# Kernel optimization log

Hardware: AMD Instinct MI355X
Metric: run time of the kernel (lower is better)

## Reference

```python
import jax, jax.numpy as jnp
import numpy as np
from jax.scipy.special import logsumexp

B = 2048       # anchors
P = 4          # positives per anchor (constant -> ragged list collapses to [B,P])
D = 256        # embed dim
N_NEG = 32768  # shared negative bank
TEMPERATURE = 0.05
ALPHA = 0.1
EPS = 1e-12    # F.normalize eps


def _l2norm(x):
    n = jnp.sqrt(jnp.sum(x * x, axis=-1, keepdims=True))
    return x / jnp.maximum(n, EPS)


def setup_inputs() -> dict:
    key = jax.random.key(0)
    k1, k2, k3 = jax.random.split(key, 3)
    return {
        "anchor_embeddings": jax.random.normal(k1, (B, D), jnp.float32),
        "positive_embeddings": jax.random.normal(k2, (B * P, D), jnp.float32),
        "negative_embeddings": jax.random.normal(k3, (N_NEG, D), jnp.float32),
        "num_positives_per_anchor": jnp.full((B,), P, dtype=jnp.int32),
    }


def reference(anchor_embeddings, positive_embeddings, negative_embeddings,
              num_positives_per_anchor):
    a = _l2norm(anchor_embeddings)                       # [B, D]
    p = _l2norm(positive_embeddings).reshape(B, P, D)    # [B, P, D]
    n = _l2norm(negative_embeddings)                     # [N, D]

    pos_sim = jnp.einsum("bd,bpd->bp", a, p) / TEMPERATURE   # [B, P]
    neg_sim = jnp.einsum("bd,nd->bn", a, n) / TEMPERATURE    # [B, N]  (dominant traffic)
    neg_lse = logsumexp(neg_sim, axis=1)                     # [B]

    # per-(anchor, positive) CE with label 0 over logits [pos_j, neg_sim_i]:
    # loss = logsumexp([pos_j, neg...]) - pos_j = logaddexp(pos_j, neg_lse_i) - pos_j
    pair_loss = jnp.logaddexp(pos_sim, neg_lse[:, None]) - pos_sim   # [B, P]
    counts = num_positives_per_anchor
    pair_mask = jnp.arange(P)[None, :] < counts[:, None]             # [B, P]
    total = jnp.sum(jnp.where(pair_mask, pair_loss, 0.0))

    # weighted-positive term (only for anchors with num_pos > 1)
    w = jax.nn.softmax(pos_sim, axis=1)                  # [B, P]
    wps = jnp.sum(w * pos_sim, axis=1)                   # [B]
    wloss = jnp.logaddexp(wps, neg_lse) - wps            # [B]
    total = total + ALPHA * jnp.sum(jnp.where(counts > 1, wloss, 0.0))

    return total / B
```

## Files before the change

### kernel.cpp

```cpp
#include <hip/hip_runtime.h>
#include <math.h>

constexpr int   B       = 2048;
constexpr int   P       = 4;
constexpr int   D       = 256;
constexpr int   NNEG    = 32768;
constexpr int   NTILES  = NNEG / 64;
constexpr float TEMP    = 0.05f;
constexpr float ALPHA   = 0.1f;
constexpr float EPS     = 1e-12f;
constexpr float INV_T   = 1.0f / TEMP;
constexpr float SCALE_Q = 28.853900817779268f;

typedef float f32x4 __attribute__((ext_vector_type(4)));
typedef int   i32x8 __attribute__((ext_vector_type(8)));

__device__ inline unsigned short f2bf(float f) {
  unsigned int u = __float_as_uint(f);
  u = (u + 0x7fffu + ((u >> 16) & 1u)) >> 16;
  return (unsigned short)u;
}
__device__ inline float bf2f(unsigned short u) {
  return __uint_as_float((unsigned int)u << 16);
}

__device__ inline float ror16_add(float v) {
  int x;
  x = __builtin_amdgcn_update_dpp(0, __float_as_int(v), 0x121, 0xf, 0xf, true);
  v += __int_as_float(x);
  x = __builtin_amdgcn_update_dpp(0, __float_as_int(v), 0x122, 0xf, 0xf, true);
  v += __int_as_float(x);
  x = __builtin_amdgcn_update_dpp(0, __float_as_int(v), 0x124, 0xf, 0xf, true);
  v += __int_as_float(x);
  x = __builtin_amdgcn_update_dpp(0, __float_as_int(v), 0x128, 0xf, 0xf, true);
  v += __int_as_float(x);
  return v;
}


constexpr int NPANEL = (B + NNEG) / 16;
constexpr int LSTR   = 264;

__global__ __launch_bounds__(256) void prep_kernel(
    const float* __restrict__ a,
    const float* __restrict__ pzx,
    const float* __restrict__ n,
    unsigned char* __restrict__ a_f8,
    unsigned char* __restrict__ n_f8,
    float* __restrict__ pos_sim,
    float* __restrict__ loss_acc,
    unsigned int* __restrict__ ticket) {
  if (blockIdx.x == 0 && threadIdx.x == 0) { *loss_acc = 0.0f; *ticket = 0u; }
  const int id   = blockIdx.x;
  const int tid  = threadIdx.x;
  const int wave = tid >> 6;
  const int lane = tid & 63;

  if (id < NPANEL) {
    __shared__ __align__(16) unsigned short sm[16 * LSTR];
    const bool isA = (id < B / 16);
    const float* src; unsigned char* dst; int prow; float post;
    if (isA) { src = a; dst = a_f8; prow = id;          post = SCALE_Q; }
    else     { src = n; dst = n_f8; prow = id - B / 16; post = 1.0f; }

#pragma unroll
    for (int rr = 0; rr < 4; rr++) {
      const int r = wave * 4 + rr;
      float4 v = ((const float4*)(src + ((size_t)prow * 16 + r) * D))[lane];
      float ss = v.x * v.x + v.y * v.y + v.z * v.z + v.w * v.w;
#pragma unroll
      for (int off = 32; off > 0; off >>= 1) ss += __shfl_xor(ss, off, 64);
      float inv = post / fmaxf(sqrtf(ss), EPS);
      ushort4 o;
      o.x = f2bf(v.x * inv); o.y = f2bf(v.y * inv);
      o.z = f2bf(v.z * inv); o.w = f2bf(v.w * inv);
      *(ushort4*)&sm[r * LSTR + lane * 4] = o;
    }
    __syncthreads();

    const int o = tid * 16;
    int r, k0;
    if (isA) {
      r  = (o >> 4) & 15;
      k0 = (o >> 11) * 128 + ((o >> 8) & 3) * 32 + ((o >> 10) & 1) * 16;
    } else {
      r  = (o >> 5) & 15;
      k0 = (o >> 11) * 128 + ((o >> 9) & 3) * 32 + (o & 16);
    }
    const unsigned short* s1 = &sm[r * LSTR + k0];
    uint4 ov;
    {
      int w0 = __builtin_amdgcn_cvt_pk_fp8_f32(bf2f(s1[0]),  bf2f(s1[1]),  0,  false);
      w0     = __builtin_amdgcn_cvt_pk_fp8_f32(bf2f(s1[2]),  bf2f(s1[3]),  w0, true);
      int w1 = __builtin_amdgcn_cvt_pk_fp8_f32(bf2f(s1[4]),  bf2f(s1[5]),  0,  false);
      w1     = __builtin_amdgcn_cvt_pk_fp8_f32(bf2f(s1[6]),  bf2f(s1[7]),  w1, true);
      int w2 = __builtin_amdgcn_cvt_pk_fp8_f32(bf2f(s1[8]),  bf2f(s1[9]),  0,  false);
      w2     = __builtin_amdgcn_cvt_pk_fp8_f32(bf2f(s1[10]), bf2f(s1[11]), w2, true);
      int w3 = __builtin_amdgcn_cvt_pk_fp8_f32(bf2f(s1[12]), bf2f(s1[13]), 0,  false);
      w3     = __builtin_amdgcn_cvt_pk_fp8_f32(bf2f(s1[14]), bf2f(s1[15]), w3, true);
      ov.x = (unsigned)w0; ov.y = (unsigned)w1;
      ov.z = (unsigned)w2; ov.w = (unsigned)w3;
    }
    *(uint4*)(dst + (size_t)prow * 4096 + tid * 16) = ov;
  } else {
    int pw = (id - NPANEL) * 4 + wave;
    if (pw >= B * P) return;
    int b = pw >> 2;
    float4 av = ((const float4*)(a + (size_t)b * D))[lane];
    float4 pv = ((const float4*)(pzx + (size_t)pw * D))[lane];
    float d  = av.x * pv.x + av.y * pv.y + av.z * pv.z + av.w * pv.w;
    float sa = av.x * av.x + av.y * av.y + av.z * av.z + av.w * av.w;
    float sp = pv.x * pv.x + pv.y * pv.y + pv.z * pv.z + pv.w * pv.w;
#pragma unroll
    for (int off = 32; off > 0; off >>= 1) {
      d  += __shfl_xor(d, off, 64);
      sa += __shfl_xor(sa, off, 64);
      sp += __shfl_xor(sp, off, 64);
    }
    if (lane == 0) {
      float inva = 1.0f / fmaxf(sqrtf(sa), EPS);
      float invp = 1.0f / fmaxf(sqrtf(sp), EPS);
      pos_sim[pw] = d * inva * invp * INV_T;
    }
  }
}

__global__ __launch_bounds__(512, 4) void negsim_mfma_kernel(
    const unsigned char* __restrict__ Af,
    const unsigned char* __restrict__ Nf,
    float* __restrict__ part_s) {
  __shared__ __align__(16) unsigned char As[4 * 4096];
  __shared__ float part_l[2][8][64];

  const int tid  = threadIdx.x;
  const int wave = tid >> 6;
  const int lane = tid & 63;

  const int id     = blockIdx.x;
  const int ngroup = id & 15;
  const int mblk   = id >> 4;
  const int m0     = mblk * 64;

#pragma unroll
  for (int t = 0; t < 2; t++) {
    const int s = wave * 2 + t;
    __builtin_amdgcn_global_load_lds(
        (const __attribute__((address_space(1))) unsigned int*)
            (Af + (size_t)(m0 >> 4) * 4096 + s * 1024 + lane * 16),
        (__attribute__((address_space(3))) unsigned int*)(As + s * 1024 + lane * 16),
        16, 0, 0);
  }

  const unsigned char* Bw = Nf + (size_t)(ngroup * 128 + wave * 2) * 4096 + lane * 32;

  i32x8 bfP0 = *(const i32x8*)(Bw);
  i32x8 bfP1 = *(const i32x8*)(Bw + 4096);
  i32x8 bfP2 = *(const i32x8*)(Bw + 2048);
  i32x8 bfP3 = *(const i32x8*)(Bw + 4096 + 2048);

  __syncthreads();

  const int aoff = lane * 16;

#define DO_ITER(B0, B1, B2, B3, PB, ITEXPR)                                    \
  {                                                                            \
    f32x4 acc[4][2] = {};                                                      \
    _Pragma("unroll")                                                          \
    for (int mi = 0; mi < 4; mi++) {                                           \
      int4 lo = *(const int4*)&As[mi * 4096 + aoff];                           \
      int4 hi = *(const int4*)&As[mi * 4096 + 1024 + aoff];                    \
      i32x8 af;                                                                \
      af[0] = lo.x; af[1] = lo.y; af[2] = lo.z; af[3] = lo.w;                  \
      af[4] = hi.x; af[5] = hi.y; af[6] = hi.z; af[7] = hi.w;                  \
      acc[mi][0] = __builtin_amdgcn_mfma_scale_f32_16x16x128_f8f6f4(           \
          af, B0, acc[mi][0], 0, 0, 0, 0x7f7f7f7f, 0, 0x7f7f7f7f);             \
      acc[mi][1] = __builtin_amdgcn_mfma_scale_f32_16x16x128_f8f6f4(           \
          af, B1, acc[mi][1], 0, 0, 0, 0x7f7f7f7f, 0, 0x7f7f7f7f);             \
    }                                                                          \
    _Pragma("unroll")                                                          \
    for (int mi = 0; mi < 4; mi++) {                                           \
      int4 lo = *(const int4*)&As[mi * 4096 + 2048 + aoff];                    \
      int4 hi = *(const int4*)&As[mi * 4096 + 2048 + 1024 + aoff];             \
      i32x8 af;                                                                \
      af[0] = lo.x; af[1] = lo.y; af[2] = lo.z; af[3] = lo.w;                  \
      af[4] = hi.x; af[5] = hi.y; af[6] = hi.z; af[7] = hi.w;                  \
      acc[mi][0] = __builtin_amdgcn_mfma_scale_f32_16x16x128_f8f6f4(           \
          af, B2, acc[mi][0], 0, 0, 0, 0x7f7f7f7f, 0, 0x7f7f7f7f);             \
      acc[mi][1] = __builtin_amdgcn_mfma_scale_f32_16x16x128_f8f6f4(           \
          af, B3, acc[mi][1], 0, 0, 0, 0x7f7f7f7f, 0, 0x7f7f7f7f);             \
    }                                                                          \
    _Pragma("unroll")                                                          \
    for (int mi = 0; mi < 4; mi++) {                                           \
      _Pragma("unroll")                                                        \
      for (int rr = 0; rr < 4; rr++) {                                         \
        float e = __builtin_amdgcn_exp2f(acc[mi][0][rr]) +                     \
                  __builtin_amdgcn_exp2f(acc[mi][1][rr]);                      \
        e = ror16_add(e);                                                      \
        if ((lane & 15) == 0)                                                  \
          part_l[PB][wave][mi * 16 + (lane >> 4) * 4 + rr] = e;                \
      }                                                                        \
    }                                                                          \
    asm volatile("s_waitcnt lgkmcnt(0)" ::: "memory");                         \
    __builtin_amdgcn_sched_barrier(0);                                         \
    __builtin_amdgcn_s_barrier();                                              \
    __builtin_amdgcn_sched_barrier(0);                                         \
    if (tid < 256) {                                                           \
      const int u4  = tid >> 6;                                                \
      const int row = tid & 63;                                                \
      float s64 = part_l[PB][2 * u4][row] + part_l[PB][2 * u4 + 1][row];       \
      part_s[(size_t)(m0 + row) * NTILES + (ngroup * 32 + (ITEXPR) * 4 + u4)]  \
          = s64;                                                               \
    }                                                                          \
  }

#pragma unroll 1
  for (int t = 0; t < 4; t++) {
    const int it0 = 2 * t;
    const unsigned char* Bq  = Bw + (size_t)(it0 + 1) * 16 * 4096;
    const unsigned char* Bpn = Bw + (size_t)((it0 + 2) & 7) * 16 * 4096;

    i32x8 bfQ0 = *(const i32x8*)(Bq);
    i32x8 bfQ1 = *(const i32x8*)(Bq + 4096);
    i32x8 bfQ2 = *(const i32x8*)(Bq + 2048);
    i32x8 bfQ3 = *(const i32x8*)(Bq + 4096 + 2048);

    DO_ITER(bfP0, bfP1, bfP2, bfP3, 0, it0)

    bfP0 = *(const i32x8*)(Bpn);
    bfP1 = *(const i32x8*)(Bpn + 4096);
    bfP2 = *(const i32x8*)(Bpn + 2048);
    bfP3 = *(const i32x8*)(Bpn + 4096 + 2048);

    DO_ITER(bfQ0, bfQ1, bfQ2, bfQ3, 1, it0 + 1)
  }
#undef DO_ITER
}

__global__ void loss_kernel(const float* __restrict__ part_s,
                            const float* __restrict__ pos_sim,
                            const int* __restrict__ counts,
                            float* __restrict__ loss_acc,
                            unsigned int* __restrict__ ticket,
                            float* __restrict__ out) {
  const int tid = threadIdx.x;
  const int b   = blockIdx.x * 16 + (tid >> 4);
  const int sub = tid & 15;
  const float* ps = part_s + (size_t)b * NTILES;
  float s = 0.0f;
#pragma unroll
  for (int i = 0; i < NTILES / 16; i++) s += ps[sub + i * 16];
  s += __shfl_xor(s, 1, 64);
  s += __shfl_xor(s, 2, 64);
  s += __shfl_xor(s, 4, 64);
  s += __shfl_xor(s, 8, 64);

  float acc = 0.0f;
  if (sub == 0) {
    float L = logf(s);
    float p0 = pos_sim[b * P + 0], p1 = pos_sim[b * P + 1];
    float p2 = pos_sim[b * P + 2], p3 = pos_sim[b * P + 3];
    int cnt = counts[b];
    float pj[P] = {p0, p1, p2, p3};
#pragma unroll
    for (int jj = 0; jj < P; jj++) {
      if (jj < cnt) {
        float hi = fmaxf(pj[jj], L), lo = fminf(pj[jj], L);
        acc += hi + log1pf(__expf(lo - hi)) - pj[jj];
      }
    }
    float mp = fmaxf(fmaxf(p0, p1), fmaxf(p2, p3));
    float e0 = __expf(p0 - mp), e1 = __expf(p1 - mp);
    float e2 = __expf(p2 - mp), e3 = __expf(p3 - mp);
    float se = e0 + e1 + e2 + e3;
    float wps = (e0 * p0 + e1 * p1 + e2 * p2 + e3 * p3) / se;
    if (cnt > 1) {
      float hi = fmaxf(wps, L), lo = fminf(wps, L);
      acc += ALPHA * (hi + log1pf(__expf(lo - hi)) - wps);
    }
  }
#pragma unroll
  for (int off = 32; off > 0; off >>= 1) acc += __shfl_xor(acc, off, 64);
  __shared__ float sa[4];
  int wid = tid >> 6, lane = tid & 63;
  if (lane == 0) sa[wid] = acc;
  __syncthreads();
  if (tid == 0) {
    atomicAdd(loss_acc, sa[0] + sa[1] + sa[2] + sa[3]);
    __threadfence();
    unsigned int t = atomicAdd(ticket, 1u);
    if (t == (unsigned int)gridDim.x - 1u) {
      float total = atomicAdd(loss_acc, 0.0f);
      out[0] = total / (float)B;
    }
  }
}

extern "C" void kernel_launch(void* const* d_in, const int* in_sizes, int n_in,
                              void* d_out, int out_size, void* d_ws,
                              size_t ws_size, hipStream_t stream) {
  const float* anc    = (const float*)d_in[0];
  const float* pos    = (const float*)d_in[1];
  const float* neg    = (const float*)d_in[2];
  const int*   counts = (const int*)d_in[3];
  float* out = (float*)d_out;

  unsigned char* a_f8 = (unsigned char*)d_ws;
  unsigned char* n_f8 = a_f8 + (size_t)B * D;
  float* part_s  = (float*)(n_f8 + (size_t)NNEG * D);
  float* pos_sim = part_s + (size_t)B * NTILES;
  float* loss_acc = pos_sim + B * P;
  unsigned int* ticket = (unsigned int*)(loss_acc + 1);

  prep_kernel<<<NPANEL + B * P / 4, 256, 0, stream>>>(
      anc, pos, neg, a_f8, n_f8, pos_sim, loss_acc, ticket);

  negsim_mfma_kernel<<<512, 512, 0, stream>>>(a_f8, n_f8, part_s);

  loss_kernel<<<B / 16, 256, 0, stream>>>(part_s, pos_sim, counts,
                                          loss_acc, ticket, out);
}
```

Measured before the change: 123.9 us.

## Keep anchor fragments in registers and drop LDS reduction barriers in negsim kernel

The anchor FP8 layout now matches the negative layout, so each wave loads its A fragments directly from global memory into registers instead of staging them through LDS. The per-iteration LDS cross-wave reduction and block barrier are removed. Each wave writes its own 32-column partial sums straight to part_s, which doubles the partial-sum buffer and the work done by loss_kernel. Grid is halved, each block covers twice as many negatives, and the launch bound drops to 2 blocks per CU to make room for the extra registers. The cost is higher register pressure and more global stores.

```diff
diff --git a/kernel.cpp b/kernel.cpp
--- a/kernel.cpp
+++ b/kernel.cpp
@@ -5,7 +5,7 @@
 constexpr int   P       = 4;
 constexpr int   D       = 256;
 constexpr int   NNEG    = 32768;
-constexpr int   NTILES  = NNEG / 64;
+constexpr int   NTILES  = NNEG / 32;
 constexpr float TEMP    = 0.05f;
 constexpr float ALPHA   = 0.1f;
 constexpr float EPS     = 1e-12f;
@@ -58,10 +58,9 @@
 
   if (id < NPANEL) {
     __shared__ __align__(16) unsigned short sm[16 * LSTR];
-    const bool isA = (id < B / 16);
     const float* src; unsigned char* dst; int prow; float post;
-    if (isA) { src = a; dst = a_f8; prow = id;          post = SCALE_Q; }
-    else     { src = n; dst = n_f8; prow = id - B / 16; post = 1.0f; }
+    if (id < B / 16) { src = a; dst = a_f8; prow = id;          post = SCALE_Q; }
+    else             { src = n; dst = n_f8; prow = id - B / 16; post = 1.0f; }
 
 #pragma unroll
     for (int rr = 0; rr < 4; rr++) {
@@ -78,15 +77,9 @@
     }
     __syncthreads();
 
-    const int o = tid * 16;
-    int r, k0;
-    if (isA) {
-      r  = (o >> 4) & 15;
-      k0 = (o >> 11) * 128 + ((o >> 8) & 3) * 32 + ((o >> 10) & 1) * 16;
-    } else {
-      r  = (o >> 5) & 15;
-      k0 = (o >> 11) * 128 + ((o >> 9) & 3) * 32 + (o & 16);
-    }
+    const int o  = tid * 16;
+    const int r  = (o >> 5) & 15;
+    const int k0 = (o >> 11) * 128 + ((o >> 9) & 3) * 32 + (o & 31);
     const unsigned short* s1 = &sm[r * LSTR + k0];
     uint4 ov;
     {
@@ -125,70 +118,56 @@
   }
 }
 
-__global__ __launch_bounds__(512, 4) void negsim_mfma_kernel(
+__global__ __launch_bounds__(512, 2) void negsim_mfma_kernel(
     const unsigned char* __restrict__ Af,
     const unsigned char* __restrict__ Nf,
     float* __restrict__ part_s) {
-  __shared__ __align__(16) unsigned char As[4 * 4096];
-  __shared__ float part_l[2][8][64];
-
   const int tid  = threadIdx.x;
   const int wave = tid >> 6;
   const int lane = tid & 63;
 
   const int id     = blockIdx.x;
-  const int ngroup = id & 15;
-  const int mblk   = id >> 4;
+  const int ngroup = id & 7;
+  const int mblk   = id >> 3;
   const int m0     = mblk * 64;
 
-#pragma unroll
-  for (int t = 0; t < 2; t++) {
-    const int s = wave * 2 + t;
-    __builtin_amdgcn_global_load_lds(
-        (const __attribute__((address_space(1))) unsigned int*)
-            (Af + (size_t)(m0 >> 4) * 4096 + s * 1024 + lane * 16),
-        (__attribute__((address_space(3))) unsigned int*)(As + s * 1024 + lane * 16),
-        16, 0, 0);
-  }
-
-  const unsigned char* Bw = Nf + (size_t)(ngroup * 128 + wave * 2) * 4096 + lane * 32;
+  const unsigned char* Ap = Af + (size_t)(m0 >> 4) * 4096 + lane * 32;
+  i32x8 af[4][2];
+#pragma unroll
+  for (int mi = 0; mi < 4; mi++)
+#pragma unroll
+    for (int h = 0; h < 2; h++)
+      af[mi][h] = *(const i32x8*)(Ap + (size_t)mi * 4096 + h * 2048);
+
+  const unsigned char* Bw =
+      Nf + (size_t)(ngroup * 256 + wave * 2) * 4096 + lane * 32;
+
+  const int rowbase = m0 + (lane >> 4) * 4;
+  const int colbase = ngroup * 128 + wave;
 
   i32x8 bfP0 = *(const i32x8*)(Bw);
   i32x8 bfP1 = *(const i32x8*)(Bw + 4096);
   i32x8 bfP2 = *(const i32x8*)(Bw + 2048);
   i32x8 bfP3 = *(const i32x8*)(Bw + 4096 + 2048);
 
-  __syncthreads();
-
-  const int aoff = lane * 16;
-
-#define DO_ITER(B0, B1, B2, B3, PB, ITEXPR)                                    \
+#define DO_ITER(B0, B1, B2, B3, ITEXPR)                                        \
   {                                                                            \
     f32x4 acc[4][2] = {};                                                      \
     _Pragma("unroll")                                                          \
     for (int mi = 0; mi < 4; mi++) {                                           \
-      int4 lo = *(const int4*)&As[mi * 4096 + aoff];                           \
-      int4 hi = *(const int4*)&As[mi * 4096 + 1024 + aoff];                    \
-      i32x8 af;                                                                \
-      af[0] = lo.x; af[1] = lo.y; af[2] = lo.z; af[3] = lo.w;                  \
-      af[4] = hi.x; af[5] = hi.y; af[6] = hi.z; af[7] = hi.w;                  \
       acc[mi][0] = __builtin_amdgcn_mfma_scale_f32_16x16x128_f8f6f4(           \
-          af, B0, acc[mi][0], 0, 0, 0, 0x7f7f7f7f, 0, 0x7f7f7f7f);             \
+          af[mi][0], B0, acc[mi][0], 0, 0, 0, 0x7f7f7f7f, 0, 0x7f7f7f7f);      \
       acc[mi][1] = __builtin_amdgcn_mfma_scale_f32_16x16x128_f8f6f4(           \
-          af, B1, acc[mi][1], 0, 0, 0, 0x7f7f7f7f, 0, 0x7f7f7f7f);             \
+          af[mi][0], B1, acc[mi][1], 0, 0, 0, 0x7f7f7f7f, 0, 0x7f7f7f7f);      \
     }                                                                          \
     _Pragma("unroll")                                                          \
     for (int mi = 0; mi < 4; mi++) {                                           \
-      int4 lo = *(const int4*)&As[mi * 4096 + 2048 + aoff];                    \
-      int4 hi = *(const int4*)&As[mi * 4096 + 2048 + 1024 + aoff];             \
-      i32x8 af;                                                                \
-      af[0] = lo.x; af[1] = lo.y; af[2] = lo.z; af[3] = lo.w;                  \
-      af[4] = hi.x; af[5] = hi.y; af[6] = hi.z; af[7] = hi.w;                  \
       acc[mi][0] = __builtin_amdgcn_mfma_scale_f32_16x16x128_f8f6f4(           \
-          af, B2, acc[mi][0], 0, 0, 0, 0x7f7f7f7f, 0, 0x7f7f7f7f);             \
+          af[mi][1], B2, acc[mi][0], 0, 0, 0, 0x7f7f7f7f, 0, 0x7f7f7f7f);      \
       acc[mi][1] = __builtin_amdgcn_mfma_scale_f32_16x16x128_f8f6f4(           \
-          af, B3, acc[mi][1], 0, 0, 0, 0x7f7f7f7f, 0, 0x7f7f7f7f);             \
+          af[mi][1], B3, acc[mi][1], 0, 0, 0, 0x7f7f7f7f, 0, 0x7f7f7f7f);      \
     }                                                                          \
+    const int col_ = colbase + (ITEXPR) * 8;                                   \
     _Pragma("unroll")                                                          \
     for (int mi = 0; mi < 4; mi++) {                                           \
       _Pragma("unroll")                                                        \
@@ -197,41 +176,30 @@
                   __builtin_amdgcn_exp2f(acc[mi][1][rr]);                      \
         e = ror16_add(e);                                                      \
         if ((lane & 15) == 0)                                                  \
-          part_l[PB][wave][mi * 16 + (lane >> 4) * 4 + rr] = e;                \
+          part_s[(size_t)(rowbase + mi * 16 + rr) * NTILES + col_] = e;        \
       }                                                                        \
     }                                                                          \
-    asm volatile("s_waitcnt lgkmcnt(0)" ::: "memory");                         \
-    __builtin_amdgcn_sched_barrier(0);                                         \
-    __builtin_amdgcn_s_barrier();                                              \
-    __builtin_amdgcn_sched_barrier(0);                                         \
-    if (tid < 256) {                                                           \
-      const int u4  = tid >> 6;                                                \
-      const int row = tid & 63;                                                \
-      float s64 = part_l[PB][2 * u4][row] + part_l[PB][2 * u4 + 1][row];       \
-      part_s[(size_t)(m0 + row) * NTILES + (ngroup * 32 + (ITEXPR) * 4 + u4)]  \
-          = s64;                                                               \
-    }                                                                          \
   }
 
 #pragma unroll 1
-  for (int t = 0; t < 4; t++) {
+  for (int t = 0; t < 8; t++) {
     const int it0 = 2 * t;
     const unsigned char* Bq  = Bw + (size_t)(it0 + 1) * 16 * 4096;
-    const unsigned char* Bpn = Bw + (size_t)((it0 + 2) & 7) * 16 * 4096;
+    const unsigned char* Bpn = Bw + (size_t)((it0 + 2) & 15) * 16 * 4096;
 
     i32x8 bfQ0 = *(const i32x8*)(Bq);
     i32x8 bfQ1 = *(const i32x8*)(Bq + 4096);
     i32x8 bfQ2 = *(const i32x8*)(Bq + 2048);
     i32x8 bfQ3 = *(const i32x8*)(Bq + 4096 + 2048);
 
-    DO_ITER(bfP0, bfP1, bfP2, bfP3, 0, it0)
+    DO_ITER(bfP0, bfP1, bfP2, bfP3, it0)
 
     bfP0 = *(const i32x8*)(Bpn);
     bfP1 = *(const i32x8*)(Bpn + 4096);
     bfP2 = *(const i32x8*)(Bpn + 2048);
     bfP3 = *(const i32x8*)(Bpn + 4096 + 2048);
 
-    DO_ITER(bfQ0, bfQ1, bfQ2, bfQ3, 1, it0 + 1)
+    DO_ITER(bfQ0, bfQ1, bfQ2, bfQ3, it0 + 1)
   }
 #undef DO_ITER
 }
@@ -314,7 +282,7 @@
   prep_kernel<<<NPANEL + B * P / 4, 256, 0, stream>>>(
       anc, pos, neg, a_f8, n_f8, pos_sim, loss_acc, ticket);
 
-  negsim_mfma_kernel<<<512, 512, 0, stream>>>(a_f8, n_f8, part_s);
+  negsim_mfma_kernel<<<256, 512, 0, stream>>>(a_f8, n_f8, part_s);
 
   loss_kernel<<<B / 16, 256, 0, stream>>>(part_s, pos_sim, counts,
                                           loss_acc, ticket, out);
```

Result: slower. 134.8 us (+8.8%).
